# Optimization experiments

Measured on AMD Instinct MI355X. Metric: run time of the kernel, lower is better.

Reference implementation:

```python
import jax, jax.numpy as jnp
import numpy as np

TAU = 1.0          # temperature
PAD = -1.0         # padded_value_indicator
MAX_ITER = 50      # sinkhorn iterations
NEG_BIG = -100000000.0


def setup_inputs() -> dict:
    key = jax.random.key(0)
    k1, k2 = jax.random.split(key)
    B, N = 128, 256
    y_pred = jax.random.normal(k1, (B, N), dtype=jnp.float32)
    y_true = jax.random.randint(k2, (B, N), 0, 5, dtype=jnp.int32)
    return {"y_pred": y_pred, "y_true": y_true}


def deterministic_neural_sort(s, tau, mask):
    # s: [B, n, 1], mask: [B, n] bool
    B, n = s.shape[0], s.shape[1]
    mor = mask[:, :, None] | mask[:, None, :]
    mand = mask[:, :, None] & mask[:, None, :]
    s = jnp.where(mask[:, :, None], NEG_BIG, s)
    A_s = jnp.abs(s - jnp.swapaxes(s, 1, 2))            # [B, n, n]
    A_s = jnp.where(mor, 0.0, A_s)
    # B_mat[b,i,j] = sum_k A_s[b,i,k] (matmul with ones outer product)
    B_mat = A_s.sum(axis=2, keepdims=True)              # [B, n, 1], broadcasts over j
    m = mask.sum(axis=1)                                # [B] number of padded items
    j = jnp.arange(n)
    valid = j[None, :] < (n - m)[:, None]
    scaling = jnp.where(
        valid,
        (n - m)[:, None].astype(jnp.float32) + 1.0 - 2.0 * (j[None, :] + 1).astype(jnp.float32),
        0.0,
    )                                                   # [B, n]
    s0 = jnp.where(mask[:, :, None], 0.0, s)
    C = s0 * scaling[:, None, :]                        # [B,n,1]*[B,1,n] outer product
    P_max = jnp.swapaxes(C - B_mat, 1, 2)
    P_max = jnp.where(mor, -jnp.inf, P_max)
    P_max = jnp.where(mand, 1.0, P_max)
    return jax.nn.softmax(P_max / tau, axis=-1)         # [B, n, n]


def sinkhorn_scaling(mat, mask):
    # mat: [B, n, n], mask: [B, n]
    mor = mask[:, None, :] | mask[:, :, None]
    mand = mask[:, None, :] & mask[:, :, None]
    mat = jnp.where(mor, 0.0, mat)
    mat = jnp.where(mand, 1.0, mat)

    def step(m, _):
        m = m / jnp.clip(m.sum(axis=1, keepdims=True), 1e-10, None)
        m = m / jnp.clip(m.sum(axis=2, keepdims=True), 1e-10, None)
        return m, None

    mat, _ = jax.lax.scan(step, mat, None, length=MAX_ITER)
    return jnp.where(mor, 0.0, mat)


def dcg_at_k(y_pred, y_true, k, gain_fn):
    # returns [B, 1]
    mask = y_true == PAD
    yp = jnp.where(mask, -jnp.inf, y_pred)
    yt = jnp.where(mask, 0.0, y_true)
    order = jnp.argsort(-yp, axis=-1)
    sorted_true = jnp.take_along_axis(yt, order, axis=-1)
    n = y_true.shape[1]
    disc = 1.0 / jnp.log2(jnp.arange(n, dtype=jnp.float32) + 2.0)
    cum = jnp.cumsum(gain_fn(sorted_true) * disc, axis=1)[:, :k]
    return cum[:, k - 1 : k]


def reference(y_pred, y_true):
    B, n = y_pred.shape
    yt = y_true.astype(jnp.float32)
    yt = yt.max() - yt + yt.min()            # relevancy flip as in source
    k = n                                    # self.k is None
    mask = yt == PAD

    P_hat = deterministic_neural_sort(y_pred[:, :, None], TAU, mask)  # [B,n,n]
    P_hat = sinkhorn_scaling(P_hat, mask)[None]                        # [1,B,n,n]
    mor = mask[None, :, :, None] | mask[None, :, None, :]
    P_hat = jnp.where(mor, 0.0, P_hat)

    yt_masked = jnp.where(mask, 0.0, yt)
    gains = jnp.power(2.0, yt_masked) - 1.0                            # powered_relevancies
    ground_truth = jnp.einsum('sbij,bj->sbi', P_hat, gains)            # [1,B,n]
    disc = 1.0 / jnp.log2(jnp.arange(n, dtype=jnp.float32) + 2.0)
    discounted_gains = ground_truth * disc

    idcg = dcg_at_k(yt, yt, k, lambda x: jnp.power(2.0, x) - 1.0).T    # [1,B]
    ndcg = discounted_gains[:, :, :k].sum(axis=-1) / (idcg + 1e-10)    # [1,B]
    idcg_mask = idcg == 0.0
    ndcg = jnp.where(idcg_mask, 0.0, ndcg)
    cnt = (~idcg_mask).sum()
    mean_ndcg = ndcg.sum() / jnp.maximum(cnt.astype(jnp.float32) * ndcg.shape[0], 1.0)
    return jnp.where(cnt > 0, -mean_ndcg, 0.0)
```

## Files before the change

kernel.cpp:

```cpp
#include <hip/hip_runtime.h>


#define NN 256
#define ITERS 50

template<int C>
__device__ __forceinline__ float dppadd(float v) {
    return v + __int_as_float(__builtin_amdgcn_update_dpp(0, __float_as_int(v), C, 0xF, 0xF, true));
}
template<int C>
__device__ __forceinline__ float dppmax(float v) {
    return fmaxf(v, __int_as_float(__builtin_amdgcn_update_dpp(0, __float_as_int(v), C, 0xF, 0xF, true)));
}
__device__ __forceinline__ float swz16(float v) {
    return __int_as_float(__builtin_amdgcn_ds_swizzle(__float_as_int(v), 0x401F));
}
__device__ __forceinline__ float sum16(float v) {
    v = dppadd<0xB1>(v);
    v = dppadd<0x4E>(v);
    v = dppadd<0x141>(v);
    v = dppadd<0x140>(v);
    return v;
}
__device__ __forceinline__ float sum32f(float v) {
    v = sum16(v);
    v += swz16(v);
    return v;
}
__device__ __forceinline__ float max32f(float v) {
    v = dppmax<0xB1>(v);
    v = dppmax<0x4E>(v);
    v = dppmax<0x141>(v);
    v = dppmax<0x140>(v);
    v = fmaxf(v, swz16(v));
    return v;
}

#if __has_builtin(__builtin_amdgcn_permlane16_swap)
#define HAVE_PLS 1
#endif

__device__ __forceinline__ void sum32_pair(float& A, float& B) {
    A = sum16(A);
    B = sum16(B);
#ifdef HAVE_PLS
    auto r1 = __builtin_amdgcn_permlane16_swap(__float_as_uint(A), __float_as_uint(B), false, false);
    float z = __uint_as_float(r1[0]) + __uint_as_float(r1[1]);
    auto r2 = __builtin_amdgcn_permlane16_swap(__float_as_uint(z), __float_as_uint(z), false, false);
    A = __uint_as_float(r2[0]);
    B = __uint_as_float(r2[1]);
#else
    A += swz16(A);
    B += swz16(B);
#endif
}

__global__ __launch_bounds__(1024, 4) void ndcg_main(const float* __restrict__ yp,
                                                     const int* __restrict__ ytr,
                                                     int nbatch,
                                                     float* __restrict__ ndOut,
                                                     float* __restrict__ cntOut) {
    const int b = blockIdx.x;
    const int t = threadIdx.x;
    const int l = t & 63;
    const int ti = t >> 5;
    const int tj = t & 31;
    const int cq = t >> 4;
    const int sl = t & 15;

    __shared__ float4 part4[32 * 64];
    __shared__ float4 cvec4[72];
    __shared__ __align__(16) float sarr[NN], bmarr[NN], garr[NN], darr[NN];
    __shared__ float numAcc, idcgAcc;
    __shared__ int hist[64], wmn[16], wmx[16], gmn, gmx;

    float* partf = (float*)part4;

    {
        int mn = 0x7fffffff, mx = (int)0x80000000;
        const int4* y4 = (const int4*)ytr;
        const int n4 = nbatch * (NN / 4);
        for (int i = t; i < n4; i += 1024) {
            int4 v = y4[i];
            mn = min(mn, min(min(v.x, v.y), min(v.z, v.w)));
            mx = max(mx, max(max(v.x, v.y), max(v.z, v.w)));
        }
        for (int mo = 1; mo < 64; mo <<= 1) {
            mn = min(mn, __shfl_xor(mn, mo));
            mx = max(mx, __shfl_xor(mx, mo));
        }
        if (l == 0) { wmn[t >> 6] = mn; wmx[t >> 6] = mx; }
    }
    if (t < 64) hist[t] = 0;
    if (t == 0) { numAcc = 0.0f; idcgAcc = 0.0f; }
    __syncthreads();
    if (t == 0) {
        int a = wmn[0], c = wmx[0];
        for (int i = 1; i < 16; ++i) { a = min(a, wmn[i]); c = max(c, wmx[i]); }
        gmn = a; gmx = c;
    }
    __syncthreads();
    const int ymin = gmn, ymax = gmx;

    if (t < NN) {
        sarr[t] = yp[b * NN + t];
        int ytv = ymax - ytr[b * NN + t] + ymin;
        garr[t] = exp2f((float)ytv) - 1.0f;
        darr[t] = 1.0f / log2f((float)t + 2.0f);
        atomicAdd(&hist[min(max(ytv - ymin, 0), 63)], 1);
    }
    __syncthreads();

    {
        int j = t & 255, q = t >> 8;
        float sv = sarr[j];
        float acc = 0.0f;
        int k0 = q * 64;
#pragma unroll 8
        for (int k = 0; k < 64; ++k) acc += fabsf(sv - sarr[k0 + k]);
        partf[q * 256 + j] = acc;
    }
    __syncthreads();
    if (t < NN)
        bmarr[t] = partf[t] + partf[256 + t] + partf[512 + t] + partf[768 + t];
    __syncthreads();

    float m[8][8];
    {
        float sj[8], bm8[8];
        *(float4*)&sj[0]  = ((const float4*)sarr)[tj * 2];
        *(float4*)&sj[4]  = ((const float4*)sarr)[tj * 2 + 1];
        *(float4*)&bm8[0] = ((const float4*)bmarr)[tj * 2];
        *(float4*)&bm8[4] = ((const float4*)bmarr)[tj * 2 + 1];
#pragma unroll
        for (int a = 0; a < 8; ++a) {
            float sc = (float)(255 - 2 * (ti * 8 + a));
            float mx = -3.0e38f;
#pragma unroll
            for (int bb = 0; bb < 8; ++bb) {
                m[a][bb] = sj[bb] * sc - bm8[bb];
                mx = fmaxf(mx, m[a][bb]);
            }
            mx = max32f(mx);
            float z = 0.0f;
#pragma unroll
            for (int bb = 0; bb < 8; ++bb) { m[a][bb] = expf(m[a][bb] - mx); z += m[a][bb]; }
            z = sum32f(z);
            float rz = __builtin_amdgcn_rcpf(z);
#pragma unroll
            for (int bb = 0; bb < 8; ++bb) m[a][bb] *= rz;
        }
    }

    if (t < NN) {
        float gain_p = 0.0f;
        int off = 0;
        for (int vb = 63; vb >= 0; --vb) {
            int c = hist[vb];
            if (t >= off && t < off + c) gain_p = exp2f((float)(vb + ymin)) - 1.0f;
            off += c;
        }
        float contrib = sum32f(darr[t] * gain_p);
        contrib += __shfl_xor(contrib, 32);
        if (l == 0) atomicAdd(&idcgAcc, contrib);
    }

    float r[8];
#pragma unroll
    for (int a = 0; a < 8; ++a) r[a] = 1.0f;

    const int wslot = ti * 64 + ((tj + ti) & 31);
    const int csc = t >> 5;
    const int hh = cq & 1;
    const int rslot1 = sl * 64 + ((csc + sl) & 31) + 32 * hh;
    const int rslot2 = (sl + 16) * 64 + ((csc + sl + 16) & 31) + 32 * hh;
    const int cwslot = cq + (cq >> 3);
    const int crslot = tj * 2 + (tj >> 2);

    {
        float p[8];
#pragma unroll
        for (int bb = 0; bb < 8; ++bb)
            p[bb] = ((m[0][bb] + m[1][bb]) + (m[2][bb] + m[3][bb])) +
                    ((m[4][bb] + m[5][bb]) + (m[6][bb] + m[7][bb]));
        part4[wslot]      = make_float4(p[0], p[1], p[2], p[3]);
        part4[wslot + 32] = make_float4(p[4], p[5], p[6], p[7]);
    }

    for (int it = 0; it < ITERS; ++it) {
        __syncthreads();
        {
            float4 A0 = part4[rslot1];
            float4 A1 = part4[rslot2];
            float4 S = make_float4(A0.x + A1.x, A0.y + A1.y, A0.z + A1.z, A0.w + A1.w);
            S.x = sum16(S.x); S.y = sum16(S.y); S.z = sum16(S.z); S.w = sum16(S.w);
            if (sl == 0) {
                float4 F;
                F.x = (S.x < 1e-10f) ? 1e10f : __builtin_amdgcn_rcpf(S.x);
                F.y = (S.y < 1e-10f) ? 1e10f : __builtin_amdgcn_rcpf(S.y);
                F.z = (S.z < 1e-10f) ? 1e10f : __builtin_amdgcn_rcpf(S.z);
                F.w = (S.w < 1e-10f) ? 1e10f : __builtin_amdgcn_rcpf(S.w);
                cvec4[cwslot] = F;
            }
        }
        __syncthreads();

        {
            float4 ca = cvec4[crslot];
            float4 cb = cvec4[crslot + 1];
            float cv[8] = {ca.x, ca.y, ca.z, ca.w, cb.x, cb.y, cb.z, cb.w};
            float rs[8];
#pragma unroll
            for (int a = 0; a < 8; ++a) {
                float acc = 0.0f;
#pragma unroll
                for (int bb = 0; bb < 8; ++bb) {
                    m[a][bb] *= cv[bb];
                    acc += m[a][bb];
                }
                rs[a] = acc;
            }
            sum32_pair(rs[0], rs[1]);
            sum32_pair(rs[2], rs[3]);
            sum32_pair(rs[4], rs[5]);
            sum32_pair(rs[6], rs[7]);
#pragma unroll
            for (int a = 0; a < 8; ++a) {
                float T = r[a] * rs[a];
                r[a] = (T < 1e-10f) ? r[a] * 1e10f : r[a] * __builtin_amdgcn_rcpf(T);
            }
            float p[8];
#pragma unroll
            for (int bb = 0; bb < 8; ++bb) {
                float acc = m[0][bb] * r[0];
#pragma unroll
                for (int a = 1; a < 8; ++a) acc = fmaf(m[a][bb], r[a], acc);
                p[bb] = acc;
            }
            part4[wslot]      = make_float4(p[0], p[1], p[2], p[3]);
            part4[wslot + 32] = make_float4(p[4], p[5], p[6], p[7]);
        }
    }

    {
        float gv[8];
        *(float4*)&gv[0] = ((const float4*)garr)[tj * 2];
        *(float4*)&gv[4] = ((const float4*)garr)[tj * 2 + 1];
        float q[8];
#pragma unroll
        for (int a = 0; a < 8; ++a) {
            float acc = m[a][0] * gv[0];
#pragma unroll
            for (int bb = 1; bb < 8; ++bb) acc = fmaf(m[a][bb], gv[bb], acc);
            q[a] = acc;
        }
        sum32_pair(q[0], q[1]);
        sum32_pair(q[2], q[3]);
        sum32_pair(q[4], q[5]);
        sum32_pair(q[6], q[7]);
        float partial = 0.0f;
#pragma unroll
        for (int a = 0; a < 8; ++a)
            partial = fmaf(darr[ti * 8 + a] * r[a], q[a], partial);
        if (tj == 0) atomicAdd(&numAcc, partial);
    }
    __syncthreads();

    if (t == 0) {
        float idcg = idcgAcc;
        bool ok = (idcg != 0.0f);
        ndOut[b] = ok ? numAcc / (idcg + 1e-10f) : 0.0f;
        cntOut[b] = ok ? 1.0f : 0.0f;
    }
}

__global__ void finalize_kernel(const float* __restrict__ ndArr,
                                const float* __restrict__ cntArr,
                                int nbatch, float* __restrict__ out) {
    int t = threadIdx.x;
    float s = 0.0f, c = 0.0f;
    for (int i = t; i < nbatch; i += 128) { s += ndArr[i]; c += cntArr[i]; }
    for (int mo = 1; mo < 64; mo <<= 1) { s += __shfl_xor(s, mo); c += __shfl_xor(c, mo); }
    __shared__ float s2[2], c2[2];
    if ((t & 63) == 0) { s2[t >> 6] = s; c2[t >> 6] = c; }
    __syncthreads();
    if (t == 0) {
        float S = s2[0] + s2[1], C = c2[0] + c2[1];
        out[0] = (C > 0.0f) ? -(S / fmaxf(C, 1.0f)) : 0.0f;
    }
}

extern "C" void kernel_launch(void* const* d_in, const int* in_sizes, int n_in,
                              void* d_out, int out_size, void* d_ws, size_t ws_size,
                              hipStream_t stream) {
    const float* y_pred = (const float*)d_in[0];
    const int* y_true = (const int*)d_in[1];
    const int total = in_sizes[0];
    const int B = total / NN;

    float* ndArr = (float*)d_ws;
    float* cntArr = ndArr + B;

    ndcg_main<<<B, 1024, 0, stream>>>(y_pred, y_true, B, ndArr, cntArr);
    finalize_kernel<<<1, 128, 0, stream>>>(ndArr, cntArr, B, (float*)d_out);
}
```

Measured before the change: 174.1 us.

## Keep column scalings implicit and fold final reduction into main kernel

```diff
diff --git a/kernel.cpp b/kernel.cpp
--- a/kernel.cpp
+++ b/kernel.cpp
@@ -58,8 +58,10 @@
 __global__ __launch_bounds__(1024, 4) void ndcg_main(const float* __restrict__ yp,
                                                      const int* __restrict__ ytr,
                                                      int nbatch,
-                                                     float* __restrict__ ndOut,
-                                                     float* __restrict__ cntOut) {
+                                                     float* __restrict__ ndArr,
+                                                     float* __restrict__ cntArr,
+                                                     int* __restrict__ doneCnt,
+                                                     float* __restrict__ out) {
     const int b = blockIdx.x;
     const int t = threadIdx.x;
     const int l = t & 63;
@@ -73,6 +75,8 @@
     __shared__ __align__(16) float sarr[NN], bmarr[NN], garr[NN], darr[NN];
     __shared__ float numAcc, idcgAcc;
     __shared__ int hist[64], wmn[16], wmx[16], gmn, gmx;
+    __shared__ float redS[16], redC[16];
+    __shared__ int lastFlag;
 
     float* partf = (float*)part4;
 
@@ -92,6 +96,7 @@
         if (l == 0) { wmn[t >> 6] = mn; wmx[t >> 6] = mx; }
     }
     if (t < 64) hist[t] = 0;
+    if (t < 72) cvec4[t] = make_float4(1.0f, 1.0f, 1.0f, 1.0f);
     if (t == 0) { numAcc = 0.0f; idcgAcc = 0.0f; }
     __syncthreads();
     if (t == 0) {
@@ -195,11 +200,13 @@
             float4 S = make_float4(A0.x + A1.x, A0.y + A1.y, A0.z + A1.z, A0.w + A1.w);
             S.x = sum16(S.x); S.y = sum16(S.y); S.z = sum16(S.z); S.w = sum16(S.w);
             if (sl == 0) {
+                float4 C = cvec4[cwslot];
+                float sx = C.x * S.x, sy = C.y * S.y, sz = C.z * S.z, sw = C.w * S.w;
                 float4 F;
-                F.x = (S.x < 1e-10f) ? 1e10f : __builtin_amdgcn_rcpf(S.x);
-                F.y = (S.y < 1e-10f) ? 1e10f : __builtin_amdgcn_rcpf(S.y);
-                F.z = (S.z < 1e-10f) ? 1e10f : __builtin_amdgcn_rcpf(S.z);
-                F.w = (S.w < 1e-10f) ? 1e10f : __builtin_amdgcn_rcpf(S.w);
+                F.x = (sx < 1e-10f) ? C.x * 1e10f : C.x * __builtin_amdgcn_rcpf(sx);
+                F.y = (sy < 1e-10f) ? C.y * 1e10f : C.y * __builtin_amdgcn_rcpf(sy);
+                F.z = (sz < 1e-10f) ? C.z * 1e10f : C.z * __builtin_amdgcn_rcpf(sz);
+                F.w = (sw < 1e-10f) ? C.w * 1e10f : C.w * __builtin_amdgcn_rcpf(sw);
                 cvec4[cwslot] = F;
             }
         }
@@ -212,12 +219,9 @@
             float rs[8];
 #pragma unroll
             for (int a = 0; a < 8; ++a) {
-                float acc = 0.0f;
-#pragma unroll
-                for (int bb = 0; bb < 8; ++bb) {
-                    m[a][bb] *= cv[bb];
-                    acc += m[a][bb];
-                }
+                float acc = m[a][0] * cv[0];
+#pragma unroll
+                for (int bb = 1; bb < 8; ++bb) acc = fmaf(m[a][bb], cv[bb], acc);
                 rs[a] = acc;
             }
             sum32_pair(rs[0], rs[1]);
@@ -243,9 +247,14 @@
     }
 
     {
+        float4 fa = cvec4[crslot];
+        float4 fb = cvec4[crslot + 1];
+        float cf[8] = {fa.x, fa.y, fa.z, fa.w, fb.x, fb.y, fb.z, fb.w};
         float gv[8];
         *(float4*)&gv[0] = ((const float4*)garr)[tj * 2];
         *(float4*)&gv[4] = ((const float4*)garr)[tj * 2 + 1];
+#pragma unroll
+        for (int bb = 0; bb < 8; ++bb) gv[bb] *= cf[bb];
         float q[8];
 #pragma unroll
         for (int a = 0; a < 8; ++a) {
@@ -269,24 +278,29 @@
     if (t == 0) {
         float idcg = idcgAcc;
         bool ok = (idcg != 0.0f);
-        ndOut[b] = ok ? numAcc / (idcg + 1e-10f) : 0.0f;
-        cntOut[b] = ok ? 1.0f : 0.0f;
-    }
-}
-
-__global__ void finalize_kernel(const float* __restrict__ ndArr,
-                                const float* __restrict__ cntArr,
-                                int nbatch, float* __restrict__ out) {
-    int t = threadIdx.x;
-    float s = 0.0f, c = 0.0f;
-    for (int i = t; i < nbatch; i += 128) { s += ndArr[i]; c += cntArr[i]; }
-    for (int mo = 1; mo < 64; mo <<= 1) { s += __shfl_xor(s, mo); c += __shfl_xor(c, mo); }
-    __shared__ float s2[2], c2[2];
-    if ((t & 63) == 0) { s2[t >> 6] = s; c2[t >> 6] = c; }
-    __syncthreads();
-    if (t == 0) {
-        float S = s2[0] + s2[1], C = c2[0] + c2[1];
-        out[0] = (C > 0.0f) ? -(S / fmaxf(C, 1.0f)) : 0.0f;
+        float nd = ok ? numAcc / (idcg + 1e-10f) : 0.0f;
+        __hip_atomic_store(&ndArr[b], nd, __ATOMIC_RELAXED, __HIP_MEMORY_SCOPE_AGENT);
+        __hip_atomic_store(&cntArr[b], ok ? 1.0f : 0.0f, __ATOMIC_RELAXED, __HIP_MEMORY_SCOPE_AGENT);
+        __threadfence();
+        int prev = atomicAdd(doneCnt, 1);
+        lastFlag = (prev == nbatch - 1) ? 1 : 0;
+    }
+    __syncthreads();
+    if (lastFlag != 0) {
+        __threadfence();
+        float s = 0.0f, c = 0.0f;
+        for (int i = t; i < nbatch; i += 1024) {
+            s += __hip_atomic_load(&ndArr[i], __ATOMIC_RELAXED, __HIP_MEMORY_SCOPE_AGENT);
+            c += __hip_atomic_load(&cntArr[i], __ATOMIC_RELAXED, __HIP_MEMORY_SCOPE_AGENT);
+        }
+        for (int mo = 1; mo < 64; mo <<= 1) { s += __shfl_xor(s, mo); c += __shfl_xor(c, mo); }
+        if (l == 0) { redS[t >> 6] = s; redC[t >> 6] = c; }
+        __syncthreads();
+        if (t == 0) {
+            float S = 0.0f, C = 0.0f;
+            for (int i = 0; i < 16; ++i) { S += redS[i]; C += redC[i]; }
+            out[0] = (C > 0.0f) ? -(S / fmaxf(C, 1.0f)) : 0.0f;
+        }
     }
 }
 
@@ -298,9 +312,11 @@
     const int total = in_sizes[0];
     const int B = total / NN;
 
-    float* ndArr = (float*)d_ws;
+    int* doneCnt = (int*)d_ws;
+    float* ndArr = (float*)d_ws + 64;
     float* cntArr = ndArr + B;
 
-    ndcg_main<<<B, 1024, 0, stream>>>(y_pred, y_true, B, ndArr, cntArr);
-    finalize_kernel<<<1, 128, 0, stream>>>(ndArr, cntArr, B, (float*)d_out);
-}
+    hipMemsetAsync(doneCnt, 0, sizeof(int), stream);
+    ndcg_main<<<B, 1024, 0, stream>>>(y_pred, y_true, B, ndArr, cntArr, doneCnt,
+                                      (float*)d_out);
+}
```

New measurement: 167.8 us. -3.6%, faster.
